# Kernel optimization log

Hardware: AMD Instinct MI355X
Metric: run time of the kernel (lower is better)

## Reference

```python
import jax, jax.numpy as jnp
import numpy as np

REGION = 64  # region_size r

def setup_inputs() -> dict:
    key = jax.random.key(0)
    B, C, H, W, k, r, T = 16, 64, 256, 256, 3, REGION, 32
    k0, k1, k2, k3, k4 = jax.random.split(key, 5)
    x = jax.random.normal(k0, (B, C, H, W), dtype=jnp.float32)
    weight = jax.random.normal(k1, (C, C, k, k), dtype=jnp.float32) * 0.05  # [out,in,kh,kw]
    h_idx = jax.random.randint(k2, (T,), 0, H - r + 1, dtype=jnp.int32)
    w_idx = jax.random.randint(k3, (T,), 0, W - r + 1, dtype=jnp.int32)
    lambdas = jax.random.uniform(k4, (T,), dtype=jnp.float32)
    return {"x": x, "weight": weight, "h_idx": h_idx, "w_idx": w_idx, "lambdas": lambdas}

def reference(x, weight, h_idx, w_idx, lambdas):
    B, C, H, W = x.shape
    k = weight.shape[-1]
    r = REGION
    n_r = (H // r) * (W // r)
    out_r = r - k + 1  # conv 'VALID' output size per region

    def step(out, t):
        h, w, lam = t
        crop = jax.lax.dynamic_slice(x, (0, 0, h, w), (B, C, r, r))
        c = jax.lax.conv_general_dilated(
            crop, weight, window_strides=(1, 1), padding='VALID',
            dimension_numbers=('NCHW', 'OIHW', 'NCHW'))
        cur = jax.lax.dynamic_slice(out, (0, 0, h, w), (B, C, out_r, out_r))
        out = jax.lax.dynamic_update_slice(out, cur + lam * c, (0, 0, h, w))
        return out, None

    out, _ = jax.lax.scan(step, jnp.zeros_like(x), (h_idx, w_idx, lambdas))
    return out / n_r
```

## Files before the change

kernel.cpp:

```cpp
#include <hip/hip_runtime.h>


typedef short short8 __attribute__((ext_vector_type(8)));
typedef float floatx4 __attribute__((ext_vector_type(4)));
typedef unsigned int uint4v __attribute__((ext_vector_type(4)));

#define OUTR 62

__device__ inline unsigned f2bf_pack(float lo, float hi) {
    unsigned ul = __builtin_bit_cast(unsigned, lo);
    unsigned uh = __builtin_bit_cast(unsigned, hi);
    ul = (ul + 0x7FFFu + ((ul >> 16) & 1u)) >> 16;
    uh = (uh + 0x7FFFu + ((uh >> 16) & 1u)) >> 16;
    return ul | (uh << 16);
}

__global__ void srconv_coeff_kernel(const int* __restrict__ h_idx,
                                    const int* __restrict__ w_idx,
                                    const float* __restrict__ lam,
                                    int T, float* __restrict__ coeff) {
    int p = blockIdx.x;
    int q = threadIdx.x;
    float c = 0.f;
    for (int t = 0; t < T; ++t) {
        int dh = p - h_idx[t];
        int dw = q - w_idx[t];
        if (dh >= 0 && dh < OUTR && dw >= 0 && dw < OUTR) c += lam[t];
    }
    coeff[(p << 8) + q] = c * (1.0f / 16.0f);
}

__global__ void srconv_wtrans_kernel(const float* __restrict__ wgt,
                                     uint4v* __restrict__ afrag) {
    int id = blockIdx.x * 256 + threadIdx.x;
    int l  = id & 63;
    int fi = id >> 6;
    int m  = fi & 3;
    int cb = (fi >> 2) & 1;
    int kk = fi >> 3;
    int co  = m * 16 + (l & 15);
    int ci0 = cb * 32 + (l >> 4) * 8;
    float w[8];
#pragma unroll
    for (int j = 0; j < 8; ++j)
        w[j] = wgt[(co * 64 + ci0 + j) * 9 + kk];
    uint4v d;
    d.x = f2bf_pack(w[0], w[1]);
    d.y = f2bf_pack(w[2], w[3]);
    d.z = f2bf_pack(w[4], w[5]);
    d.w = f2bf_pack(w[6], w[7]);
    afrag[id] = d;
}

__launch_bounds__(256, 2)
__global__ void srconv_fused_kernel(const float* __restrict__ x,
                                    const float* __restrict__ coeff,
                                    const short8* __restrict__ afrag,
                                    float* __restrict__ out) {
    __shared__ __align__(16) unsigned xs[2 * 340 * 16];

    const int tid  = threadIdx.x;
    const int lane = tid & 63;
    const int wv   = tid >> 6;
    const int l15  = lane & 15;
    const int kg   = lane >> 4;

    const unsigned bid = blockIdx.x;
    const unsigned swz = (bid & 7) * 512 + (bid >> 3);
    const int b    = swz >> 8;
    const int tile = swz & 255;
    const int P0   = (tile >> 3) << 3;
    const int Q0   = (tile & 7) << 5;

    float myc = coeff[((P0 + (tid >> 5)) << 8) + Q0 + (tid & 31)];
    if (__syncthreads_count(myc != 0.f) == 0) {
        const floatx4 z = (floatx4){0.f, 0.f, 0.f, 0.f};
        for (int u = tid; u < 64 * 8 * 8; u += 256) {
            int q4 = u & 7;
            int pr = (u >> 3) & 7;
            int co = u >> 6;
            *(floatx4*)(out + (((b << 6) + co) << 16) +
                        ((P0 + pr) << 8) + Q0 + (q4 << 2)) = z;
        }
        return;
    }

    const int prb = P0 + (wv << 1);

    float cf[2][2];
#pragma unroll
    for (int p = 0; p < 2; ++p)
#pragma unroll
        for (int h = 0; h < 2; ++h)
            cf[p][h] = coeff[((prb + p) << 8) + Q0 + (h << 4) + l15];

    const float* xb = x + ((size_t)b << 22);

    floatx4 va[6][2], vb[6][2];

#pragma unroll
    for (int r = 0; r < 6; ++r) {
        int u  = r * 256 + tid;
        int uc = u < 1440 ? u : 1439;
        int cp    = uc / 90;
        int rem   = uc - cp * 90;
        int row   = rem / 9;
        int chunk = rem - row * 9;
        int gr    = min(P0 + row, 255);
        int gcb   = min(Q0 + (chunk << 2), 252);
        const float* xp = xb + (cp << 17) + (gr << 8) + gcb;
        va[r][0] = *(const floatx4*)(xp);
        va[r][1] = *(const floatx4*)(xp + 65536);
    }

    short8 areg[2][4];
#pragma unroll
    for (int m = 0; m < 4; ++m) {
        areg[0][m] = afrag[(0 + m) * 64 + lane];
        areg[1][m] = afrag[(8 + m) * 64 + lane];
    }

#pragma unroll
    for (int r = 0; r < 6; ++r) {
        int u  = r * 256 + tid;
        int uc = u < 1440 ? u : 1439;
        int cp    = uc / 90;
        int rem   = uc - cp * 90;
        int row   = rem / 9;
        int chunk = rem - row * 9;
        int gr    = min(P0 + row, 255);
        int gcb   = min(Q0 + (chunk << 2), 252);
        const float* xp = xb + ((16 + cp) << 17) + (gr << 8) + gcb;
        vb[r][0] = *(const floatx4*)(xp);
        vb[r][1] = *(const floatx4*)(xp + 65536);
    }

#pragma unroll
    for (int r = 0; r < 6; ++r) {
        int u  = r * 256 + tid;
        int uc = u < 1440 ? u : 1439;
        int cp    = uc / 90;
        int rem   = uc - cp * 90;
        int row   = rem / 9;
        int chunk = rem - row * 9;
        int c4 = chunk << 2;
#pragma unroll
        for (int j = 0; j < 4; ++j) {
            if (u < 1440 && c4 + j < 34) {
                int pix = row * 34 + c4 + j;
                int slot = cp ^ (((pix >> 1) & 3) << 2);
                xs[(pix << 4) + slot] = f2bf_pack(va[r][0][j], va[r][1][j]);
            }
        }
    }
    __syncthreads();

    floatx4 acc[4][2][2];
#pragma unroll
    for (int m = 0; m < 4; ++m)
#pragma unroll
        for (int p = 0; p < 2; ++p)
#pragma unroll
            for (int h = 0; h < 2; ++h)
                acc[m][p][h] = (floatx4){0.f, 0.f, 0.f, 0.f};

#pragma unroll 2
    for (int t = 0; t < 9; ++t) {
        const int kh = t / 3;
        const int kw = t - kh * 3;
        const int cur = t & 1;

        short8 bf[2][2];
#pragma unroll
        for (int p = 0; p < 2; ++p)
#pragma unroll
            for (int h = 0; h < 2; ++h) {
                int prl = (wv << 1) + p + kh;
                int cl  = (h << 4) + l15 + kw;
                int pix = prl * 34 + cl;
                int off = (pix << 4) +
                          ((kg << 2) ^ (((pix >> 1) & 3) << 2));
                bf[p][h] = *(const short8*)(&xs[off]);
            }
        __builtin_amdgcn_s_setprio(1);
#pragma unroll
        for (int m = 0; m < 4; ++m)
#pragma unroll
            for (int p = 0; p < 2; ++p)
#pragma unroll
                for (int h = 0; h < 2; ++h)
                    acc[m][p][h] = __builtin_amdgcn_mfma_f32_16x16x32_bf16(
                        areg[cur][m], bf[p][h], acc[m][p][h], 0, 0, 0);
        __builtin_amdgcn_s_setprio(0);

        {
            const int tn  = t + 2;
            const int cbn = tn / 9;
            const int kkn = tn - cbn * 9;
#pragma unroll
            for (int m = 0; m < 4; ++m)
                areg[cur][m] =
                    afrag[((((kkn << 1) + cbn) << 2) + m) * 64 + lane];
        }
    }

#pragma unroll
    for (int r = 0; r < 6; ++r) {
        int u  = r * 256 + tid;
        int uc = u < 1440 ? u : 1439;
        int cp    = uc / 90;
        int rem   = uc - cp * 90;
        int row   = rem / 9;
        int chunk = rem - row * 9;
        int c4 = chunk << 2;
#pragma unroll
        for (int j = 0; j < 4; ++j) {
            if (u < 1440 && c4 + j < 34) {
                int pix = row * 34 + c4 + j;
                int slot = cp ^ (((pix >> 1) & 3) << 2);
                xs[5440 + (pix << 4) + slot] =
                    f2bf_pack(vb[r][0][j], vb[r][1][j]);
            }
        }
    }
    __syncthreads();

#pragma unroll 2
    for (int t = 9; t < 18; ++t) {
        const int kk = t - 9;
        const int kh = kk / 3;
        const int kw = kk - kh * 3;
        const int cur = t & 1;

        short8 bf[2][2];
#pragma unroll
        for (int p = 0; p < 2; ++p)
#pragma unroll
            for (int h = 0; h < 2; ++h) {
                int prl = (wv << 1) + p + kh;
                int cl  = (h << 4) + l15 + kw;
                int pix = prl * 34 + cl;
                int off = 5440 + (pix << 4) +
                          ((kg << 2) ^ (((pix >> 1) & 3) << 2));
                bf[p][h] = *(const short8*)(&xs[off]);
            }
        __builtin_amdgcn_s_setprio(1);
#pragma unroll
        for (int m = 0; m < 4; ++m)
#pragma unroll
            for (int p = 0; p < 2; ++p)
#pragma unroll
                for (int h = 0; h < 2; ++h)
                    acc[m][p][h] = __builtin_amdgcn_mfma_f32_16x16x32_bf16(
                        areg[cur][m], bf[p][h], acc[m][p][h], 0, 0, 0);
        __builtin_amdgcn_s_setprio(0);

        if (t < 16) {
            const int tn  = t + 2;
            const int kkn = tn - 9;
#pragma unroll
            for (int m = 0; m < 4; ++m)
                areg[cur][m] =
                    afrag[((((kkn << 1) + 1) << 2) + m) * 64 + lane];
        }
    }
    __syncthreads();

    float* epb = reinterpret_cast<float*>(xs);
    const int co_l = lane >> 3;
    const int q4   = lane & 7;

#pragma unroll
    for (int p = 0; p < 2; ++p) {
        const int pr = prb + p;
#pragma unroll
        for (int m = 0; m < 4; ++m) {
            float* ep = epb + (((wv << 1) + (m & 1)) * 576);
#pragma unroll
            for (int h = 0; h < 2; ++h)
#pragma unroll
                for (int reg = 0; reg < 4; ++reg)
                    ep[((kg << 2) + reg) * 36 + (h << 4) + l15] =
                        acc[m][p][h][reg] * cf[p][h];
#pragma unroll
            for (int j = 0; j < 2; ++j) {
                const floatx4 v = *reinterpret_cast<const floatx4*>(
                    &ep[(co_l + (j << 3)) * 36 + (q4 << 2)]);
                const int co = (m << 4) + co_l + (j << 3);
                *(floatx4*)(out + (((b << 6) + co) << 16) +
                            (pr << 8) + Q0 + (q4 << 2)) = v;
            }
        }
    }
}

extern "C" void kernel_launch(void* const* d_in, const int* in_sizes, int n_in,
                              void* d_out, int out_size, void* d_ws, size_t ws_size,
                              hipStream_t stream) {
    const float* x     = (const float*)d_in[0];
    const float* wgt   = (const float*)d_in[1];
    const int*   h_idx = (const int*)d_in[2];
    const int*   w_idx = (const int*)d_in[3];
    const float* lam   = (const float*)d_in[4];
    float*       out   = (float*)d_out;
    float*       coeff = (float*)d_ws;
    char*        af_b  = (char*)d_ws + 65536 * sizeof(float);
    const int    T     = in_sizes[2];

    srconv_coeff_kernel<<<256, 256, 0, stream>>>(h_idx, w_idx, lam, T, coeff);
    srconv_wtrans_kernel<<<18, 256, 0, stream>>>(wgt, (uint4v*)af_b);
    srconv_fused_kernel<<<4096, 256, 0, stream>>>(
        x, coeff, (const short8*)af_b, out);
}
```

Measured before the change: 172.2 us.

## Stage weight fragments through LDS per channel half instead of per-step global loads

```diff
diff --git a/kernel.cpp b/kernel.cpp
--- a/kernel.cpp
+++ b/kernel.cpp
@@ -55,9 +55,10 @@
 __launch_bounds__(256, 2)
 __global__ void srconv_fused_kernel(const float* __restrict__ x,
                                     const float* __restrict__ coeff,
-                                    const short8* __restrict__ afrag,
+                                    const uint4v* __restrict__ afrag,
                                     float* __restrict__ out) {
     __shared__ __align__(16) unsigned xs[2 * 340 * 16];
+    __shared__ __align__(16) uint4v af_lds[2304];
 
     const int tid  = threadIdx.x;
     const int lane = tid & 63;
@@ -97,7 +98,13 @@
     const float* xb = x + ((size_t)b << 22);
 
     floatx4 va[6][2], vb[6][2];
-
+    uint4v  vc[9];
+
+#pragma unroll
+    for (int i = 0; i < 9; ++i) {
+        int e = i * 256 + tid;
+        vc[i] = afrag[e + ((e >> 8) << 8)];
+    }
 #pragma unroll
     for (int r = 0; r < 6; ++r) {
         int u  = r * 256 + tid;
@@ -113,11 +120,26 @@
         va[r][1] = *(const floatx4*)(xp + 65536);
     }
 
-    short8 areg[2][4];
-#pragma unroll
-    for (int m = 0; m < 4; ++m) {
-        areg[0][m] = afrag[(0 + m) * 64 + lane];
-        areg[1][m] = afrag[(8 + m) * 64 + lane];
+#pragma unroll
+    for (int i = 0; i < 9; ++i)
+        af_lds[i * 256 + tid] = vc[i];
+#pragma unroll
+    for (int r = 0; r < 6; ++r) {
+        int u  = r * 256 + tid;
+        int uc = u < 1440 ? u : 1439;
+        int cp    = uc / 90;
+        int rem   = uc - cp * 90;
+        int row   = rem / 9;
+        int chunk = rem - row * 9;
+        int c4 = chunk << 2;
+#pragma unroll
+        for (int j = 0; j < 4; ++j) {
+            if (u < 1440 && c4 + j < 34) {
+                int pix = row * 34 + c4 + j;
+                int slot = cp ^ (((pix >> 1) & 3) << 2);
+                xs[(pix << 4) + slot] = f2bf_pack(va[r][0][j], va[r][1][j]);
+            }
+        }
     }
 
 #pragma unroll
@@ -134,6 +156,56 @@
         vb[r][0] = *(const floatx4*)(xp);
         vb[r][1] = *(const floatx4*)(xp + 65536);
     }
+#pragma unroll
+    for (int i = 0; i < 9; ++i) {
+        int e = i * 256 + tid;
+        vc[i] = afrag[e + ((e >> 8) << 8) + 256];
+    }
+    __syncthreads();
+
+    floatx4 acc[4][2][2];
+#pragma unroll
+    for (int m = 0; m < 4; ++m)
+#pragma unroll
+        for (int p = 0; p < 2; ++p)
+#pragma unroll
+            for (int h = 0; h < 2; ++h)
+                acc[m][p][h] = (floatx4){0.f, 0.f, 0.f, 0.f};
+
+#pragma unroll 2
+    for (int t = 0; t < 9; ++t) {
+        const int kh = t / 3;
+        const int kw = t - kh * 3;
+
+        short8 a[4];
+#pragma unroll
+        for (int m = 0; m < 4; ++m)
+            a[m] = *reinterpret_cast<const short8*>(
+                &af_lds[(t << 8) + (m << 6) + lane]);
+        short8 bf[2][2];
+#pragma unroll
+        for (int p = 0; p < 2; ++p)
+#pragma unroll
+            for (int h = 0; h < 2; ++h) {
+                int prl = (wv << 1) + p + kh;
+                int cl  = (h << 4) + l15 + kw;
+                int pix = prl * 34 + cl;
+                int off = (pix << 4) +
+                          ((kg << 2) ^ (((pix >> 1) & 3) << 2));
+                bf[p][h] = *(const short8*)(&xs[off]);
+            }
+        __builtin_amdgcn_s_setprio(1);
+#pragma unroll
+        for (int m = 0; m < 4; ++m)
+#pragma unroll
+            for (int p = 0; p < 2; ++p)
+#pragma unroll
+                for (int h = 0; h < 2; ++h)
+                    acc[m][p][h] = __builtin_amdgcn_mfma_f32_16x16x32_bf16(
+                        a[m], bf[p][h], acc[m][p][h], 0, 0, 0);
+        __builtin_amdgcn_s_setprio(0);
+    }
+    __syncthreads();
 
 #pragma unroll
     for (int r = 0; r < 6; ++r) {
@@ -149,89 +221,26 @@
             if (u < 1440 && c4 + j < 34) {
                 int pix = row * 34 + c4 + j;
                 int slot = cp ^ (((pix >> 1) & 3) << 2);
-                xs[(pix << 4) + slot] = f2bf_pack(va[r][0][j], va[r][1][j]);
+                xs[5440 + (pix << 4) + slot] =
+                    f2bf_pack(vb[r][0][j], vb[r][1][j]);
             }
         }
     }
+#pragma unroll
+    for (int i = 0; i < 9; ++i)
+        af_lds[i * 256 + tid] = vc[i];
     __syncthreads();
-
-    floatx4 acc[4][2][2];
-#pragma unroll
-    for (int m = 0; m < 4; ++m)
-#pragma unroll
-        for (int p = 0; p < 2; ++p)
-#pragma unroll
-            for (int h = 0; h < 2; ++h)
-                acc[m][p][h] = (floatx4){0.f, 0.f, 0.f, 0.f};
 
 #pragma unroll 2
     for (int t = 0; t < 9; ++t) {
         const int kh = t / 3;
         const int kw = t - kh * 3;
-        const int cur = t & 1;
-
-        short8 bf[2][2];
-#pragma unroll
-        for (int p = 0; p < 2; ++p)
-#pragma unroll
-            for (int h = 0; h < 2; ++h) {
-                int prl = (wv << 1) + p + kh;
-                int cl  = (h << 4) + l15 + kw;
-                int pix = prl * 34 + cl;
-                int off = (pix << 4) +
-                          ((kg << 2) ^ (((pix >> 1) & 3) << 2));
-                bf[p][h] = *(const short8*)(&xs[off]);
-            }
-        __builtin_amdgcn_s_setprio(1);
+
+        short8 a[4];
 #pragma unroll
         for (int m = 0; m < 4; ++m)
-#pragma unroll
-            for (int p = 0; p < 2; ++p)
-#pragma unroll
-                for (int h = 0; h < 2; ++h)
-                    acc[m][p][h] = __builtin_amdgcn_mfma_f32_16x16x32_bf16(
-                        areg[cur][m], bf[p][h], acc[m][p][h], 0, 0, 0);
-        __builtin_amdgcn_s_setprio(0);
-
-        {
-            const int tn  = t + 2;
-            const int cbn = tn / 9;
-            const int kkn = tn - cbn * 9;
-#pragma unroll
-            for (int m = 0; m < 4; ++m)
-                areg[cur][m] =
-                    afrag[((((kkn << 1) + cbn) << 2) + m) * 64 + lane];
-        }
-    }
-
-#pragma unroll
-    for (int r = 0; r < 6; ++r) {
-        int u  = r * 256 + tid;
-        int uc = u < 1440 ? u : 1439;
-        int cp    = uc / 90;
-        int rem   = uc - cp * 90;
-        int row   = rem / 9;
-        int chunk = rem - row * 9;
-        int c4 = chunk << 2;
-#pragma unroll
-        for (int j = 0; j < 4; ++j) {
-            if (u < 1440 && c4 + j < 34) {
-                int pix = row * 34 + c4 + j;
-                int slot = cp ^ (((pix >> 1) & 3) << 2);
-                xs[5440 + (pix << 4) + slot] =
-                    f2bf_pack(vb[r][0][j], vb[r][1][j]);
-            }
-        }
-    }
-    __syncthreads();
-
-#pragma unroll 2
-    for (int t = 9; t < 18; ++t) {
-        const int kk = t - 9;
-        const int kh = kk / 3;
-        const int kw = kk - kh * 3;
-        const int cur = t & 1;
-
+            a[m] = *reinterpret_cast<const short8*>(
+                &af_lds[(t << 8) + (m << 6) + lane]);
         short8 bf[2][2];
 #pragma unroll
         for (int p = 0; p < 2; ++p)
@@ -252,17 +261,8 @@
 #pragma unroll
                 for (int h = 0; h < 2; ++h)
                     acc[m][p][h] = __builtin_amdgcn_mfma_f32_16x16x32_bf16(
-                        areg[cur][m], bf[p][h], acc[m][p][h], 0, 0, 0);
+                        a[m], bf[p][h], acc[m][p][h], 0, 0, 0);
         __builtin_amdgcn_s_setprio(0);
-
-        if (t < 16) {
-            const int tn  = t + 2;
-            const int kkn = tn - 9;
-#pragma unroll
-            for (int m = 0; m < 4; ++m)
-                areg[cur][m] =
-                    afrag[((((kkn << 1) + 1) << 2) + m) * 64 + lane];
-        }
     }
     __syncthreads();
 
@@ -310,5 +310,5 @@
     srconv_coeff_kernel<<<256, 256, 0, stream>>>(h_idx, w_idx, lam, T, coeff);
     srconv_wtrans_kernel<<<18, 256, 0, stream>>>(wgt, (uint4v*)af_b);
     srconv_fused_kernel<<<4096, 256, 0, stream>>>(
-        x, coeff, (const short8*)af_b, out);
-}
+        x, coeff, (const uint4v*)af_b, out);
+}
```

Measured after the change: 169.8 us (median of 3 runs). No clear change (-1.4%).
